# Kernel tuning notes

Measured on AMD Instinct MI355X. Metric: run time of the kernel, lower is better.

The kernel has to match this reference:

```python
import jax, jax.numpy as jnp
import numpy as np

B, V, CODE_NUM = 64, 100, 4096
CODE_SIZE, ATT, VISIT, TIME, HID, OUT = 256, 128, 256, 64, 512, 90
TYPE_NUM = 32
NEG = -2.0 ** 31


def setup_inputs() -> dict:
    key = jax.random.key(0)
    ks = jax.random.split(key, 24)
    s = 0.02
    return {
        'code_x': jax.random.randint(ks[0], (B, V, CODE_NUM), 0, 2).astype(jnp.float32),
        'code_type0': jax.random.randint(ks[1], (CODE_NUM + 1,), 0, TYPE_NUM),
        'code_type1': jax.random.randint(ks[2], (CODE_NUM + 1,), 0, TYPE_NUM),
        'code_type2': jax.random.randint(ks[3], (CODE_NUM + 1,), 0, TYPE_NUM),
        'lens': jax.random.randint(ks[4], (B,), 1, V + 1),
        'intervals': jax.random.uniform(ks[5], (B, V), dtype=jnp.float32),
        # encoder: code + 3 type embedding tables (rows 1..code_num used)
        'code_emb': jax.random.normal(ks[6], (CODE_NUM + 1, CODE_SIZE), jnp.float32) * s,
        't0_emb': jax.random.normal(ks[7], (TYPE_NUM, CODE_SIZE), jnp.float32) * s,
        't1_emb': jax.random.normal(ks[8], (TYPE_NUM, CODE_SIZE), jnp.float32) * s,
        't2_emb': jax.random.normal(ks[9], (TYPE_NUM, CODE_SIZE), jnp.float32) * s,
        # visit self-attention (no bias, per nn.Linear(..., bias=False))
        'Wq': jax.random.normal(ks[10], (CODE_SIZE, ATT), jnp.float32) * s,
        'Wk': jax.random.normal(ks[11], (CODE_SIZE, ATT), jnp.float32) * s,
        'Wv': jax.random.normal(ks[12], (CODE_SIZE, VISIT), jnp.float32) * s,
        # time embedding Linear(1, time_size)
        'time_w': jax.random.normal(ks[13], (TIME,), jnp.float32) * s,
        'time_b': jnp.zeros((TIME,), jnp.float32),
        # GRUCell params (torch layout: gates ordered r,z,n)
        'gru_Wih': jax.random.normal(ks[14], (3 * HID, VISIT + TIME), jnp.float32) * s,
        'gru_Whh': jax.random.normal(ks[15], (3 * HID, HID), jnp.float32) * s,
        'gru_bih': jnp.zeros((3 * HID,), jnp.float32),
        'gru_bhh': jnp.zeros((3 * HID,), jnp.float32),
        # classifier
        'cls_W': jax.random.normal(ks[16], (OUT, HID), jnp.float32) * s,
        'cls_b': jnp.zeros((OUT,), jnp.float32),
    }


def reference(code_x, code_type0, code_type1, code_type2, lens, intervals,
              code_emb, t0_emb, t1_emb, t2_emb, Wq, Wk, Wv, time_w, time_b,
              gru_Wih, gru_Whh, gru_bih, gru_bhh, cls_W, cls_b):
    # --- Encoder (vectorized): multi-hot slot i corresponds to code id i+1 ---
    E = (code_emb[1:]
         + t0_emb[code_type0[1:]]
         + t1_emb[code_type1[1:]]
         + t2_emb[code_type2[1:]])                      # [CODE_NUM, CODE_SIZE]
    active = (code_x > 0).astype(E.dtype)               # [B, V, CODE_NUM]
    counts = jnp.maximum(active.sum(-1, keepdims=True), 1.0)
    v_emb_ini = jnp.einsum('bvc,cd->bvd', active, E) / counts  # mean over codes
    visit_mask = jnp.arange(V)[None, :] < lens[:, None]        # [B, V]
    v_emb_ini = v_emb_ini * visit_mask[..., None]              # padded visits stay 0

    # --- Context-aware visit self-attention ---
    Q = v_emb_ini @ Wq                                   # [B, V, ATT]
    K = v_emb_ini @ Wk
    Vv = v_emb_ini @ Wv                                  # [B, V, VISIT]
    alpha = jnp.einsum('bqa,bka->bqk', Q, K)
    alpha = jnp.where(visit_mask[:, None, :], alpha, NEG)  # mask keys
    alpha = jax.nn.softmax(alpha, axis=2)
    v_emb = jnp.einsum('bqk,bkd->bqd', alpha, Vv) + Vv     # [B, V, VISIT]

    # --- Time-aware input ---
    t_emb = intervals[..., None] * time_w + time_b         # [B, V, TIME]
    x = jnp.concatenate([v_emb, t_emb], axis=-1)           # [B, V, VISIT+TIME]

    # --- GRU over visits, gated by per-patient length ---
    def step(h, xm):
        xt, mt = xm                                        # xt [B,D], mt [B]
        gi = xt @ gru_Wih.T + gru_bih
        gh = h @ gru_Whh.T + gru_bhh
        ir, iz, inn = jnp.split(gi, 3, axis=-1)
        hr, hz, hn = jnp.split(gh, 3, axis=-1)
        r = jax.nn.sigmoid(ir + hr)
        z = jax.nn.sigmoid(iz + hz)
        n = jnp.tanh(inn + r * hn)
        h_new = (1.0 - z) * n + z * h
        h = jnp.where(mt[:, None], h_new, h)
        return h, None

    h0 = jnp.zeros((B, HID), x.dtype)
    h_final, _ = jax.lax.scan(step, h0, (x.transpose(1, 0, 2), visit_mask.T))

    # --- Classifier (dropout p=0 -> identity) ---
    return jax.nn.sigmoid(h_final @ cls_W.T + cls_b)       # [B, OUT]
```

## Files before the change

### kernel.cpp

```cpp
#include <hip/hip_runtime.h>
#include <hip/hip_bf16.h>

typedef float  f32x4 __attribute__((ext_vector_type(4)));
typedef short  s16x8 __attribute__((ext_vector_type(8)));

#define NEGBIG -1e30f

__device__ __forceinline__ unsigned short f2b(float f) {
    union { float f; unsigned u; } c; c.f = f;
    unsigned r = c.u + 0x7FFF + ((c.u >> 16) & 1);
    return (unsigned short)(r >> 16);
}
__device__ __forceinline__ float b2f(unsigned short h) {
    union { unsigned u; float f; } c; c.u = ((unsigned)h) << 16;
    return c.f;
}
__device__ __forceinline__ float sigm(float x) { return 1.f / (1.f + __expf(-x)); }

__device__ __forceinline__ s16x8 ld_b128_sc(const unsigned short* p) {
    s16x8 r;
    asm volatile("global_load_dwordx4 %0, %1, off sc0 sc1" : "=v"(r) : "v"(p));
    return r;
}
__device__ __forceinline__ void st_short_sc(unsigned short* p, unsigned short v) {
    unsigned int dv = v;
    asm volatile("global_store_short %0, %1, off sc0 sc1" :: "v"(p), "v"(dv) : "memory");
}
__device__ __forceinline__ void st_dword_sc(float* p, float v) {
    asm volatile("global_store_dword %0, %1, off sc0 sc1" :: "v"(p), "v"(v) : "memory");
}

__global__ void init_zero(int* flags, unsigned short* hb0) {
    int t = threadIdx.x;
    for (int i = t; i < 1024; i += 256) flags[i] = 0;
    for (int i = t; i < 32768; i += 256) hb0[i] = 0;
}

__global__ void prep_w(const float* Wq, const float* Wk, const float* Wv,
                       const float* gWih, const float* gWhh,
                       unsigned short* wcat, unsigned short* wih, unsigned short* whh) {
    int idx = blockIdx.x * 256 + threadIdx.x;
    int stride = gridDim.x * 256;
    const int N1 = 131072, N2 = 491520, N3 = 786432;
    for (; idx < N1 + N2 + N3; idx += stride) {
        if (idx < N1) {
            int n = idx >> 8, k = idx & 255;
            float v;
            if (n < 128) v = Wq[k * 128 + n];
            else if (n < 256) v = Wk[k * 128 + (n - 128)];
            else v = Wv[k * 256 + (n - 256)];
            wcat[n * 256 + k] = f2b(v);
        } else if (idx < N1 + N2) {
            int i = idx - N1; wih[i] = f2b(gWih[i]);
        } else {
            int i = idx - N1 - N2; whh[i] = f2b(gWhh[i]);
        }
    }
}

__global__ __launch_bounds__(256) void prep_et(const float* code_emb, const int* ct0, const int* ct1, const int* ct2,
                                               const float* t0e, const float* t1e, const float* t2e,
                                               unsigned short* ET) {
    __shared__ float tile[64][65];
    const int d0 = blockIdx.x * 64, c0 = blockIdx.y * 64;
    const int t = threadIdx.x;
    for (int p = 0; p < 16; ++p) {
        int idx = p * 256 + t;
        int dl = idx & 63, cl = idx >> 6;
        int code = c0 + cl + 1;
        int d = d0 + dl;
        float v = code_emb[code * 256 + d] + t0e[ct0[code] * 256 + d]
                + t1e[ct1[code] * 256 + d] + t2e[ct2[code] * 256 + d];
        tile[dl][cl] = v;
    }
    __syncthreads();
    for (int p = 0; p < 2; ++p) {
        int idx = p * 256 + t;
        int dl = idx >> 3, ch = idx & 7;
        s16x8 pk;
#pragma unroll
        for (int e = 0; e < 8; ++e) pk[e] = (short)f2b(tile[dl][ch * 8 + e]);
        *(s16x8*)(ET + (size_t)(d0 + dl) * 4096 + c0 + ch * 8) = pk;
    }
}

__global__ __launch_bounds__(256) void enc_gemm(const float* code_x, const unsigned short* ET,
                                                const int* lens, unsigned short* Vb) {
    __shared__ __align__(16) char sm[4096 + 32768 + 128];
    char* As = sm;
    char* Bs = sm + 4096;
    float* cl = (float*)(sm + 4096 + 32768);
    const int m0 = blockIdx.x * 32;
    const int t = threadIdx.x, l = t & 63, w = t >> 6;
    const int lr = l & 15, lq = l >> 4, l7 = l & 7;
    const int sr = t >> 3, sc = t & 7;
    f32x4 acc[2][4];
#pragma unroll
    for (int a = 0; a < 2; ++a)
#pragma unroll
        for (int b = 0; b < 4; ++b) acc[a][b] = (f32x4){0.f, 0.f, 0.f, 0.f};
    int cnt = 0;
    for (int it = 0; it < 64; ++it) {
        const int k0 = it * 64;
        const float* ga = code_x + (size_t)(m0 + sr) * 4096 + k0 + sc * 8;
        f32x4 a0 = *(const f32x4*)ga;
        f32x4 a1 = *(const f32x4*)(ga + 4);
        s16x8 ap;
#pragma unroll
        for (int e = 0; e < 4; ++e) { bool on = a0[e] > 0.f; ap[e] = on ? (short)0x3F80 : (short)0; cnt += on ? 1 : 0; }
#pragma unroll
        for (int e = 0; e < 4; ++e) { bool on = a1[e] > 0.f; ap[4 + e] = on ? (short)0x3F80 : (short)0; cnt += on ? 1 : 0; }
        *(s16x8*)(As + sr * 128 + ((sc ^ (sr & 7)) << 4)) = ap;
#pragma unroll
        for (int rd = 0; rd < 8; ++rd) {
            int i = rd * 256 + t;
            int n = i >> 3, cc = i & 7;
            s16x8 bv = *(const s16x8*)(ET + (size_t)n * 4096 + k0 + cc * 8);
            *(s16x8*)(Bs + n * 128 + ((cc ^ (n & 7)) << 4)) = bv;
        }
        __syncthreads();
#pragma unroll
        for (int kk = 0; kk < 2; ++kk) {
            const int cp = kk * 4 + lq;
            s16x8 af[2], bf[4];
#pragma unroll
            for (int mt = 0; mt < 2; ++mt)
                af[mt] = *(const s16x8*)(As + (mt * 16 + lr) * 128 + ((cp ^ l7) << 4));
#pragma unroll
            for (int nt = 0; nt < 4; ++nt)
                bf[nt] = *(const s16x8*)(Bs + ((w * 4 + nt) * 16 + lr) * 128 + ((cp ^ l7) << 4));
#pragma unroll
            for (int mt = 0; mt < 2; ++mt)
#pragma unroll
                for (int nt = 0; nt < 4; ++nt)
                    acc[mt][nt] = __builtin_amdgcn_mfma_f32_16x16x32_bf16(af[mt], bf[nt], acc[mt][nt], 0, 0, 0);
        }
        __syncthreads();
    }
    float fc = (float)cnt;
    fc += __shfl_xor(fc, 1); fc += __shfl_xor(fc, 2); fc += __shfl_xor(fc, 4);
    if (sc == 0) cl[sr] = fmaxf(fc, 1.f);
    __syncthreads();
#pragma unroll
    for (int mt = 0; mt < 2; ++mt)
#pragma unroll
        for (int i = 0; i < 4; ++i) {
            int m = mt * 16 + lq * 4 + i;
            int gm = m0 + m;
            float rc = 1.f / cl[m];
            unsigned bi = (unsigned)gm / 100u;
            unsigned vi = (unsigned)gm - bi * 100u;
            float msk = ((int)vi < lens[bi]) ? 1.f : 0.f;
#pragma unroll
            for (int nt = 0; nt < 4; ++nt) {
                int n = (w * 4 + nt) * 16 + lr;
                Vb[(size_t)gm * 256 + n] = f2b(acc[mt][nt][i] * rc * msk);
            }
        }
}

__global__ __launch_bounds__(256) void gemm_bf16(const unsigned short* A, const unsigned short* Bm,
                                                 int K, int Ntot, int mode,
                                                 unsigned short* outp, const float* bias) {
    __shared__ __align__(16) char sm[4096 + 32768];
    char* As = sm;
    char* Bs = sm + 4096;
    const int m0 = blockIdx.x * 32;
    const int n0 = blockIdx.y * 256;
    const int t = threadIdx.x, l = t & 63, w = t >> 6;
    const int lr = l & 15, lq = l >> 4, l7 = l & 7;
    const int sr = t >> 3, sc = t & 7;
    const int iters = K >> 6;
    f32x4 acc[2][4];
#pragma unroll
    for (int a = 0; a < 2; ++a)
#pragma unroll
        for (int b = 0; b < 4; ++b) acc[a][b] = (f32x4){0.f, 0.f, 0.f, 0.f};
    for (int it = 0; it < iters; ++it) {
        const int k0 = it * 64;
        s16x8 av = *(const s16x8*)(A + (size_t)(m0 + sr) * K + k0 + sc * 8);
        *(s16x8*)(As + sr * 128 + ((sc ^ (sr & 7)) << 4)) = av;
#pragma unroll
        for (int rd = 0; rd < 8; ++rd) {
            int i = rd * 256 + t;
            int n = i >> 3, cc = i & 7;
            s16x8 bv = *(const s16x8*)(Bm + (size_t)(n0 + n) * K + k0 + cc * 8);
            *(s16x8*)(Bs + n * 128 + ((cc ^ (n & 7)) << 4)) = bv;
        }
        __syncthreads();
#pragma unroll
        for (int kk = 0; kk < 2; ++kk) {
            const int cp = kk * 4 + lq;
            s16x8 af[2], bf[4];
#pragma unroll
            for (int mt = 0; mt < 2; ++mt)
                af[mt] = *(const s16x8*)(As + (mt * 16 + lr) * 128 + ((cp ^ l7) << 4));
#pragma unroll
            for (int nt = 0; nt < 4; ++nt)
                bf[nt] = *(const s16x8*)(Bs + ((w * 4 + nt) * 16 + lr) * 128 + ((cp ^ l7) << 4));
#pragma unroll
            for (int mt = 0; mt < 2; ++mt)
#pragma unroll
                for (int nt = 0; nt < 4; ++nt)
                    acc[mt][nt] = __builtin_amdgcn_mfma_f32_16x16x32_bf16(af[mt], bf[nt], acc[mt][nt], 0, 0, 0);
        }
        __syncthreads();
    }
#pragma unroll
    for (int mt = 0; mt < 2; ++mt)
#pragma unroll
        for (int i = 0; i < 4; ++i) {
            int gm = m0 + mt * 16 + lq * 4 + i;
#pragma unroll
            for (int nt = 0; nt < 4; ++nt) {
                int n = n0 + (w * 4 + nt) * 16 + lr;
                float v = acc[mt][nt][i];
                if (mode == 1) v += bias[n];
                outp[(size_t)gm * Ntot + n] = f2b(v);
            }
        }
}

__global__ __launch_bounds__(256) void attn_kernel(const unsigned short* QKV, const int* lens,
                                                   const float* intervals, const float* time_w, const float* time_b,
                                                   unsigned short* X) {
    __shared__ __align__(16) char sm[28672 + 32768];
    char* Pb = sm;
    char* VTb = sm + 28672;
    const int b = blockIdx.x;
    const int t = threadIdx.x, l = t & 63, w = t >> 6;
    const int lr = l & 15, lq = l >> 4;
    const int lenb = lens[b];
    for (int p = 0; p < 7; ++p) {
        int idx = p * 256 + t;
        *(f32x4*)(Pb + idx * 16) = (f32x4){0.f, 0.f, 0.f, 0.f};
    }
    __syncthreads();
    f32x4 S[2][7];
#pragma unroll
    for (int a = 0; a < 2; ++a)
#pragma unroll
        for (int c = 0; c < 7; ++c) S[a][c] = (f32x4){0.f, 0.f, 0.f, 0.f};
#pragma unroll
    for (int kk = 0; kk < 4; ++kk) {
        s16x8 qa[2], kb[7];
#pragma unroll
        for (int mi = 0; mi < 2; ++mi) {
            int mt = 2 * w + mi;
            if (mt > 6) continue;
            int row = b * 100 + mt * 16 + lr;
            qa[mi] = *(const s16x8*)(QKV + (size_t)row * 512 + kk * 32 + lq * 8);
        }
#pragma unroll
        for (int nt = 0; nt < 7; ++nt) {
            int row = b * 100 + nt * 16 + lr;
            kb[nt] = *(const s16x8*)(QKV + (size_t)row * 512 + 128 + kk * 32 + lq * 8);
        }
#pragma unroll
        for (int mi = 0; mi < 2; ++mi) {
            int mt = 2 * w + mi;
            if (mt > 6) continue;
#pragma unroll
            for (int nt = 0; nt < 7; ++nt)
                S[mi][nt] = __builtin_amdgcn_mfma_f32_16x16x32_bf16(qa[mi], kb[nt], S[mi][nt], 0, 0, 0);
        }
    }
#pragma unroll
    for (int mi = 0; mi < 2; ++mi) {
        int mt = 2 * w + mi;
        if (mt > 6) continue;
        float sv[7][4];
#pragma unroll
        for (int nt = 0; nt < 7; ++nt) {
            int j = nt * 16 + lr;
#pragma unroll
            for (int i = 0; i < 4; ++i)
                sv[nt][i] = (j < lenb) ? S[mi][nt][i] : NEGBIG;
        }
#pragma unroll
        for (int i = 0; i < 4; ++i) {
            float mx = sv[0][i];
#pragma unroll
            for (int nt = 1; nt < 7; ++nt) mx = fmaxf(mx, sv[nt][i]);
            mx = fmaxf(mx, __shfl_xor(mx, 1));
            mx = fmaxf(mx, __shfl_xor(mx, 2));
            mx = fmaxf(mx, __shfl_xor(mx, 4));
            mx = fmaxf(mx, __shfl_xor(mx, 8));
            float e[7], sum = 0.f;
#pragma unroll
            for (int nt = 0; nt < 7; ++nt) { e[nt] = __expf(sv[nt][i] - mx); sum += e[nt]; }
            sum += __shfl_xor(sum, 1);
            sum += __shfl_xor(sum, 2);
            sum += __shfl_xor(sum, 4);
            sum += __shfl_xor(sum, 8);
            float rs = 1.f / sum;
            int m = mt * 16 + lq * 4 + i;
#pragma unroll
            for (int nt = 0; nt < 7; ++nt) {
                int j = nt * 16 + lr;
                *(unsigned short*)(Pb + m * 256 + (((j >> 3) ^ (m & 7)) << 4) + ((j & 7) << 1)) = f2b(e[nt] * rs);
            }
        }
    }
    __syncthreads();
    for (int h = 0; h < 2; ++h) {
        for (int p = 0; p < 8; ++p) {
            int idx = p * 256 + t;
            *(f32x4*)(VTb + idx * 16) = (f32x4){0.f, 0.f, 0.f, 0.f};
        }
        __syncthreads();
        for (int p = 0; p < 7; ++p) {
            int ci = p * 256 + t;
            if (ci < 1600) {
                int j = ci >> 4, d8 = ci & 15;
                s16x8 vv = *(const s16x8*)(QKV + (size_t)(b * 100 + j) * 512 + 256 + h * 128 + d8 * 8);
#pragma unroll
                for (int e = 0; e < 8; ++e) {
                    int dl = d8 * 8 + e;
                    *(unsigned short*)(VTb + dl * 256 + (((j >> 3) ^ (dl & 7)) << 4) + ((j & 7) << 1)) = (unsigned short)vv[e];
                }
            }
        }
        __syncthreads();
        f32x4 O[2][8];
#pragma unroll
        for (int a = 0; a < 2; ++a)
#pragma unroll
            for (int c = 0; c < 8; ++c) O[a][c] = (f32x4){0.f, 0.f, 0.f, 0.f};
#pragma unroll
        for (int kk = 0; kk < 4; ++kk) {
            s16x8 pa[2];
#pragma unroll
            for (int mi = 0; mi < 2; ++mi) {
                int mt = 2 * w + mi;
                if (mt > 6) continue;
                int m = mt * 16 + lr;
                pa[mi] = *(const s16x8*)(Pb + m * 256 + (((kk * 4 + lq) ^ (m & 7)) << 4));
            }
#pragma unroll
            for (int nt = 0; nt < 8; ++nt) {
                int dl = nt * 16 + lr;
                s16x8 vb = *(const s16x8*)(VTb + dl * 256 + (((kk * 4 + lq) ^ (dl & 7)) << 4));
#pragma unroll
                for (int mi = 0; mi < 2; ++mi) {
                    int mt = 2 * w + mi;
                    if (mt > 6) continue;
                    O[mi][nt] = __builtin_amdgcn_mfma_f32_16x16x32_bf16(pa[mi], vb, O[mi][nt], 0, 0, 0);
                }
            }
        }
#pragma unroll
        for (int mi = 0; mi < 2; ++mi) {
            int mt = 2 * w + mi;
            if (mt > 6) continue;
#pragma unroll
            for (int i = 0; i < 4; ++i) {
                int m = mt * 16 + lq * 4 + i;
                if (m < 100) {
#pragma unroll
                    for (int nt = 0; nt < 8; ++nt) {
                        int dl = nt * 16 + lr;
                        float res = b2f(*(unsigned short*)(VTb + dl * 256 + (((m >> 3) ^ (dl & 7)) << 4) + ((m & 7) << 1)));
                        X[(size_t)(b * 100 + m) * 320 + h * 128 + dl] = f2b(O[mi][nt][i] + res);
                    }
                }
            }
        }
        if (h == 0) __syncthreads();
    }
    for (int p = 0; p < 25; ++p) {
        int idx = p * 256 + t;
        int m = idx >> 6, d = idx & 63;
        float val = intervals[b * 100 + m] * time_w[d] + time_b[d];
        X[(size_t)(b * 100 + m) * 320 + 256 + d] = f2b(val);
    }
}

__global__ __launch_bounds__(256, 1) void gru_kernel(const unsigned short* GIb, const unsigned short* WHH,
                                                     const float* gbhh, const int* lens,
                                                     unsigned short* hb0, unsigned short* hb1, float* hf,
                                                     int* flags, const float* clsW, const float* clsb, float* out) {
    const int bid = blockIdx.x;
    const int t = threadIdx.x, l = t & 63, w = t >> 6;
    const int lr = l & 15, lq = l >> 4;
    const int d0 = bid * 16;
    const int j = d0 + lr;
    int ml;
    {
        int v = lens[l];
        v = max(v, __shfl_xor(v, 1));  v = max(v, __shfl_xor(v, 2));
        v = max(v, __shfl_xor(v, 4));  v = max(v, __shfl_xor(v, 8));
        v = max(v, __shfl_xor(v, 16)); v = max(v, __shfl_xor(v, 32));
        ml = v;
    }
    int lens4[4];
#pragma unroll
    for (int i = 0; i < 4; ++i) lens4[i] = lens[w * 16 + lq * 4 + i];
    const float bhr = gbhh[j], bhz = gbhh[512 + j], bhn = gbhh[1024 + j];
    s16x8 Bf[3][16];
#pragma unroll
    for (int g = 0; g < 3; ++g)
#pragma unroll
        for (int kk = 0; kk < 16; ++kk)
            Bf[g][kk] = *(const s16x8*)(WHH + (size_t)(g * 512 + j) * 512 + kk * 32 + lq * 8);
    float ho[4] = {0.f, 0.f, 0.f, 0.f};
    size_t gi_base[4];
#pragma unroll
    for (int i = 0; i < 4; ++i) gi_base[i] = (size_t)((w * 16 + lq * 4 + i) * 100) * 1536 + j;

    float gir[4], giz[4], gin[4];
#pragma unroll
    for (int i = 0; i < 4; ++i) {
        const unsigned short* gp = GIb + gi_base[i];
        gir[i] = b2f(gp[0]); giz[i] = b2f(gp[512]); gin[i] = b2f(gp[1024]);
    }

    for (int step = 0; step < ml; ++step) {
        const unsigned short* hb = (step & 1) ? hb1 : hb0;
        unsigned short* hn = (step & 1) ? hb0 : hb1;
        s16x8 af[16];
#pragma unroll
        for (int kk = 0; kk < 16; ++kk)
            af[kk] = ld_b128_sc(hb + (size_t)(w * 16 + lr) * 512 + kk * 32 + lq * 8);
        asm volatile("s_waitcnt vmcnt(0)" ::: "memory");
        __builtin_amdgcn_sched_barrier(0);
        f32x4 ar = (f32x4){0.f,0.f,0.f,0.f}, az = ar, an = ar;
#pragma unroll
        for (int kk = 0; kk < 16; ++kk) {
            ar = __builtin_amdgcn_mfma_f32_16x16x32_bf16(af[kk], Bf[0][kk], ar, 0, 0, 0);
            az = __builtin_amdgcn_mfma_f32_16x16x32_bf16(af[kk], Bf[1][kk], az, 0, 0, 0);
            an = __builtin_amdgcn_mfma_f32_16x16x32_bf16(af[kk], Bf[2][kk], an, 0, 0, 0);
        }
#pragma unroll
        for (int i = 0; i < 4; ++i) {
            float r = sigm(gir[i] + ar[i] + bhr);
            float z = sigm(giz[i] + az[i] + bhz);
            float n = tanhf(gin[i] + r * (an[i] + bhn));
            float hv = (step < lens4[i]) ? ((1.f - z) * n + z * ho[i]) : ho[i];
            ho[i] = hv;
            st_short_sc(hn + (size_t)(w * 16 + lq * 4 + i) * 512 + j, f2b(hv));
        }
        asm volatile("s_waitcnt vmcnt(0)" ::: "memory");
        __syncthreads();
        if (t == 0)
            __hip_atomic_store(flags + bid * 16, step + 1, __ATOMIC_RELAXED, __HIP_MEMORY_SCOPE_AGENT);
        if (step + 1 < ml) {
#pragma unroll
            for (int i = 0; i < 4; ++i) {
                const unsigned short* gp = GIb + gi_base[i] + (size_t)(step + 1) * 1536;
                gir[i] = b2f(gp[0]); giz[i] = b2f(gp[512]); gin[i] = b2f(gp[1024]);
            }
        }
        if (w == 0) {
            int guard = 0;
            while (true) {
                int v = (l < 32) ? __hip_atomic_load(flags + l * 16, __ATOMIC_RELAXED, __HIP_MEMORY_SCOPE_AGENT) : (step + 1);
                if (__all(v >= step + 1)) break;
                if (++guard > (1 << 20)) break;
                __builtin_amdgcn_s_sleep(1);
            }
        }
        __syncthreads();
    }
#pragma unroll
    for (int i = 0; i < 4; ++i)
        st_dword_sc(hf + (size_t)(w * 16 + lq * 4 + i) * 512 + j, ho[i]);
    asm volatile("s_waitcnt vmcnt(0)" ::: "memory");
    __syncthreads();
    if (t == 0)
        __hip_atomic_store(flags + bid * 16, ml + 1, __ATOMIC_RELAXED, __HIP_MEMORY_SCOPE_AGENT);
    if (w == 0) {
        int guard = 0;
        while (true) {
            int v = (l < 32) ? __hip_atomic_load(flags + l * 16, __ATOMIC_RELAXED, __HIP_MEMORY_SCOPE_AGENT) : (ml + 1);
            if (__all(v >= ml + 1)) break;
            if (++guard > (1 << 20)) break;
            __builtin_amdgcn_s_sleep(1);
        }
    }
    __syncthreads();
    if (bid < 30) {
        int bb = t >> 2, qq = t & 3;
        int c0 = bid * 3;
        float s0 = 0.f, s1 = 0.f, s2 = 0.f;
        for (int kc = 0; kc < 32; ++kc) {
            int k = qq * 128 + kc * 4;
            f32x4 hv = *(const f32x4*)(hf + bb * 512 + k);
            f32x4 w0 = *(const f32x4*)(clsW + (c0 + 0) * 512 + k);
            f32x4 w1 = *(const f32x4*)(clsW + (c0 + 1) * 512 + k);
            f32x4 w2 = *(const f32x4*)(clsW + (c0 + 2) * 512 + k);
            s0 += hv[0] * w0[0] + hv[1] * w0[1] + hv[2] * w0[2] + hv[3] * w0[3];
            s1 += hv[0] * w1[0] + hv[1] * w1[1] + hv[2] * w1[2] + hv[3] * w1[3];
            s2 += hv[0] * w2[0] + hv[1] * w2[1] + hv[2] * w2[2] + hv[3] * w2[3];
        }
        s0 += __shfl_xor(s0, 1); s0 += __shfl_xor(s0, 2);
        s1 += __shfl_xor(s1, 1); s1 += __shfl_xor(s1, 2);
        s2 += __shfl_xor(s2, 1); s2 += __shfl_xor(s2, 2);
        if (qq == 0) {
            out[bb * 90 + c0 + 0] = sigm(s0 + clsb[c0 + 0]);
            out[bb * 90 + c0 + 1] = sigm(s1 + clsb[c0 + 1]);
            out[bb * 90 + c0 + 2] = sigm(s2 + clsb[c0 + 2]);
        }
    }
}

extern "C" void kernel_launch(void* const* d_in, const int* in_sizes, int n_in,
                              void* d_out, int out_size, void* d_ws, size_t ws_size,
                              hipStream_t stream) {
    const float* code_x   = (const float*)d_in[0];
    const int*   ct0      = (const int*)d_in[1];
    const int*   ct1      = (const int*)d_in[2];
    const int*   ct2      = (const int*)d_in[3];
    const int*   lens     = (const int*)d_in[4];
    const float* intervals= (const float*)d_in[5];
    const float* code_emb = (const float*)d_in[6];
    const float* t0e      = (const float*)d_in[7];
    const float* t1e      = (const float*)d_in[8];
    const float* t2e      = (const float*)d_in[9];
    const float* Wq       = (const float*)d_in[10];
    const float* Wk       = (const float*)d_in[11];
    const float* Wv       = (const float*)d_in[12];
    const float* time_w   = (const float*)d_in[13];
    const float* time_b   = (const float*)d_in[14];
    const float* gWih     = (const float*)d_in[15];
    const float* gWhh     = (const float*)d_in[16];
    const float* gbih     = (const float*)d_in[17];
    const float* gbhh     = (const float*)d_in[18];
    const float* clsW     = (const float*)d_in[19];
    const float* clsb     = (const float*)d_in[20];

    char* ws = (char*)d_ws;
    const size_t ET_OFF   = 0;
    const size_t WCAT_OFF = 2097152;
    const size_t WIH_OFF  = 2359296;
    const size_t WHH_OFF  = 3342336;
    const size_t V_OFF    = 4915200;
    const size_t QKV_OFF  = 8192000;
    const size_t X_OFF    = 14778368;
    const size_t GI_OFF   = 18874368;
    const size_t HB0_OFF  = 38535168;
    const size_t HB1_OFF  = 38600704;
    const size_t HF_OFF   = 38666240;
    const size_t FLG_OFF  = 38797312;

    unsigned short* ET   = (unsigned short*)(ws + ET_OFF);
    unsigned short* WCAT = (unsigned short*)(ws + WCAT_OFF);
    unsigned short* WIH  = (unsigned short*)(ws + WIH_OFF);
    unsigned short* WHH  = (unsigned short*)(ws + WHH_OFF);
    unsigned short* Vb   = (unsigned short*)(ws + V_OFF);
    unsigned short* QKV  = (unsigned short*)(ws + QKV_OFF);
    unsigned short* Xb   = (unsigned short*)(ws + X_OFF);
    unsigned short* GIb  = (unsigned short*)(ws + GI_OFF);
    unsigned short* hb0  = (unsigned short*)(ws + HB0_OFF);
    unsigned short* hb1  = (unsigned short*)(ws + HB1_OFF);
    float*          hf   = (float*)(ws + HF_OFF);
    int*            flags= (int*)(ws + FLG_OFF);

    init_zero<<<1, 256, 0, stream>>>(flags, hb0);
    prep_w<<<512, 256, 0, stream>>>(Wq, Wk, Wv, gWih, gWhh, WCAT, WIH, WHH);
    prep_et<<<dim3(4, 64), 256, 0, stream>>>(code_emb, ct0, ct1, ct2, t0e, t1e, t2e, ET);
    enc_gemm<<<200, 256, 0, stream>>>(code_x, ET, lens, Vb);
    gemm_bf16<<<dim3(200, 2), 256, 0, stream>>>(Vb, WCAT, 256, 512, 2, QKV, nullptr);
    attn_kernel<<<64, 256, 0, stream>>>(QKV, lens, intervals, time_w, time_b, Xb);
    gemm_bf16<<<dim3(200, 6), 256, 0, stream>>>(Xb, WIH, 320, 1536, 1, GIb, gbih);
    gru_kernel<<<32, 256, 0, stream>>>(GIb, WHH, gbhh, lens, hb0, hb1, hf, flags, clsW, clsb, (float*)d_out);
}
```

Before: 769.9 us.

## Prefetch GEMM tiles into registers, merge prep kernels, split attention by head

```diff
diff --git a/kernel.cpp b/kernel.cpp
--- a/kernel.cpp
+++ b/kernel.cpp
@@ -30,57 +30,59 @@
     asm volatile("global_store_dword %0, %1, off sc0 sc1" :: "v"(p), "v"(v) : "memory");
 }
 
-__global__ void init_zero(int* flags, unsigned short* hb0) {
-    int t = threadIdx.x;
-    for (int i = t; i < 1024; i += 256) flags[i] = 0;
-    for (int i = t; i < 32768; i += 256) hb0[i] = 0;
-}
-
-__global__ void prep_w(const float* Wq, const float* Wk, const float* Wv,
-                       const float* gWih, const float* gWhh,
-                       unsigned short* wcat, unsigned short* wih, unsigned short* whh) {
-    int idx = blockIdx.x * 256 + threadIdx.x;
-    int stride = gridDim.x * 256;
-    const int N1 = 131072, N2 = 491520, N3 = 786432;
-    for (; idx < N1 + N2 + N3; idx += stride) {
-        if (idx < N1) {
-            int n = idx >> 8, k = idx & 255;
-            float v;
-            if (n < 128) v = Wq[k * 128 + n];
-            else if (n < 256) v = Wk[k * 128 + (n - 128)];
-            else v = Wv[k * 256 + (n - 256)];
-            wcat[n * 256 + k] = f2b(v);
-        } else if (idx < N1 + N2) {
-            int i = idx - N1; wih[i] = f2b(gWih[i]);
-        } else {
-            int i = idx - N1 - N2; whh[i] = f2b(gWhh[i]);
-        }
-    }
-}
-
-__global__ __launch_bounds__(256) void prep_et(const float* code_emb, const int* ct0, const int* ct1, const int* ct2,
-                                               const float* t0e, const float* t1e, const float* t2e,
-                                               unsigned short* ET) {
+__global__ __launch_bounds__(256) void prep_all(const float* code_emb, const int* ct0, const int* ct1, const int* ct2,
+                                                const float* t0e, const float* t1e, const float* t2e,
+                                                const float* Wq, const float* Wk, const float* Wv,
+                                                const float* gWih, const float* gWhh,
+                                                unsigned short* ET, unsigned short* wcat,
+                                                unsigned short* wih, unsigned short* whh,
+                                                int* flags, unsigned short* hb0) {
     __shared__ float tile[64][65];
-    const int d0 = blockIdx.x * 64, c0 = blockIdx.y * 64;
+    const int bid = blockIdx.x;
     const int t = threadIdx.x;
-    for (int p = 0; p < 16; ++p) {
-        int idx = p * 256 + t;
-        int dl = idx & 63, cl = idx >> 6;
-        int code = c0 + cl + 1;
-        int d = d0 + dl;
-        float v = code_emb[code * 256 + d] + t0e[ct0[code] * 256 + d]
-                + t1e[ct1[code] * 256 + d] + t2e[ct2[code] * 256 + d];
-        tile[dl][cl] = v;
-    }
-    __syncthreads();
-    for (int p = 0; p < 2; ++p) {
-        int idx = p * 256 + t;
-        int dl = idx >> 3, ch = idx & 7;
-        s16x8 pk;
-#pragma unroll
-        for (int e = 0; e < 8; ++e) pk[e] = (short)f2b(tile[dl][ch * 8 + e]);
-        *(s16x8*)(ET + (size_t)(d0 + dl) * 4096 + c0 + ch * 8) = pk;
+    if (bid < 256) {
+        const int d0 = (bid & 3) * 64, c0 = (bid >> 2) * 64;
+        for (int p = 0; p < 16; ++p) {
+            int idx = p * 256 + t;
+            int dl = idx & 63, cl = idx >> 6;
+            int code = c0 + cl + 1;
+            int d = d0 + dl;
+            float v = code_emb[code * 256 + d] + t0e[ct0[code] * 256 + d]
+                    + t1e[ct1[code] * 256 + d] + t2e[ct2[code] * 256 + d];
+            tile[dl][cl] = v;
+        }
+        __syncthreads();
+        for (int p = 0; p < 2; ++p) {
+            int idx = p * 256 + t;
+            int dl = idx >> 3, ch = idx & 7;
+            s16x8 pk;
+#pragma unroll
+            for (int e = 0; e < 8; ++e) pk[e] = (short)f2b(tile[dl][ch * 8 + e]);
+            *(s16x8*)(ET + (size_t)(d0 + dl) * 4096 + c0 + ch * 8) = pk;
+        }
+    } else {
+        if (bid >= 504) {
+            int idx = (bid - 504) * 256 + t;
+            for (int i = idx; i < 1024; i += 2048) flags[i] = 0;
+            for (int i = idx; i < 32768; i += 2048) hb0[i] = 0;
+        }
+        int idx = (bid - 256) * 256 + t;
+        const int stride = 256 * 256;
+        const int N1 = 131072, N2 = 491520, N3 = 786432;
+        for (; idx < N1 + N2 + N3; idx += stride) {
+            if (idx < N1) {
+                int n = idx >> 8, k = idx & 255;
+                float v;
+                if (n < 128) v = Wq[k * 128 + n];
+                else if (n < 256) v = Wk[k * 128 + (n - 128)];
+                else v = Wv[k * 256 + (n - 256)];
+                wcat[n * 256 + k] = f2b(v);
+            } else if (idx < N1 + N2) {
+                int i = idx - N1; wih[i] = f2b(gWih[i]);
+            } else {
+                int i = idx - N1 - N2; whh[i] = f2b(gWhh[i]);
+            }
+        }
     }
 }
 
@@ -94,49 +96,69 @@
     const int t = threadIdx.x, l = t & 63, w = t >> 6;
     const int lr = l & 15, lq = l >> 4, l7 = l & 7;
     const int sr = t >> 3, sc = t & 7;
+    const int bn = t >> 3, bc = t & 7;
+    const float* gabase = code_x + (size_t)(m0 + sr) * 4096 + sc * 8;
     f32x4 acc[2][4];
 #pragma unroll
     for (int a = 0; a < 2; ++a)
 #pragma unroll
         for (int b = 0; b < 4; ++b) acc[a][b] = (f32x4){0.f, 0.f, 0.f, 0.f};
     int cnt = 0;
-    for (int it = 0; it < 64; ++it) {
-        const int k0 = it * 64;
-        const float* ga = code_x + (size_t)(m0 + sr) * 4096 + k0 + sc * 8;
-        f32x4 a0 = *(const f32x4*)ga;
-        f32x4 a1 = *(const f32x4*)(ga + 4);
-        s16x8 ap;
-#pragma unroll
-        for (int e = 0; e < 4; ++e) { bool on = a0[e] > 0.f; ap[e] = on ? (short)0x3F80 : (short)0; cnt += on ? 1 : 0; }
-#pragma unroll
-        for (int e = 0; e < 4; ++e) { bool on = a1[e] > 0.f; ap[4 + e] = on ? (short)0x3F80 : (short)0; cnt += on ? 1 : 0; }
-        *(s16x8*)(As + sr * 128 + ((sc ^ (sr & 7)) << 4)) = ap;
-#pragma unroll
-        for (int rd = 0; rd < 8; ++rd) {
-            int i = rd * 256 + t;
-            int n = i >> 3, cc = i & 7;
-            s16x8 bv = *(const s16x8*)(ET + (size_t)n * 4096 + k0 + cc * 8);
-            *(s16x8*)(Bs + n * 128 + ((cc ^ (n & 7)) << 4)) = bv;
-        }
-        __syncthreads();
-#pragma unroll
-        for (int kk = 0; kk < 2; ++kk) {
-            const int cp = kk * 4 + lq;
-            s16x8 af[2], bf[4];
-#pragma unroll
-            for (int mt = 0; mt < 2; ++mt)
-                af[mt] = *(const s16x8*)(As + (mt * 16 + lr) * 128 + ((cp ^ l7) << 4));
-#pragma unroll
-            for (int nt = 0; nt < 4; ++nt)
-                bf[nt] = *(const s16x8*)(Bs + ((w * 4 + nt) * 16 + lr) * 128 + ((cp ^ l7) << 4));
-#pragma unroll
-            for (int mt = 0; mt < 2; ++mt)
-#pragma unroll
-                for (int nt = 0; nt < 4; ++nt)
-                    acc[mt][nt] = __builtin_amdgcn_mfma_f32_16x16x32_bf16(af[mt], bf[nt], acc[mt][nt], 0, 0, 0);
-        }
-        __syncthreads();
-    }
+
+    f32x4 a0A, a1A, a0B, a1B;
+    s16x8 bA[8], bB[8];
+
+#define ENC_ISSUE(SLOT, IT) do {                                                     \
+    const int k0_ = (IT) * 64;                                                       \
+    a0##SLOT = *(const f32x4*)(gabase + k0_);                                        \
+    a1##SLOT = *(const f32x4*)(gabase + k0_ + 4);                                    \
+    _Pragma("unroll")                                                                \
+    for (int rd_ = 0; rd_ < 8; ++rd_)                                                \
+        b##SLOT[rd_] = *(const s16x8*)(ET + (size_t)(rd_ * 32 + bn) * 4096 + k0_ + bc * 8); \
+} while (0)
+
+#define ENC_CONSUME(SLOT, NEXTIT) do {                                               \
+    s16x8 ap_;                                                                       \
+    _Pragma("unroll")                                                                \
+    for (int e_ = 0; e_ < 4; ++e_) { bool on_ = a0##SLOT[e_] > 0.f; ap_[e_] = on_ ? (short)0x3F80 : (short)0; cnt += on_ ? 1 : 0; } \
+    _Pragma("unroll")                                                                \
+    for (int e_ = 0; e_ < 4; ++e_) { bool on_ = a1##SLOT[e_] > 0.f; ap_[4 + e_] = on_ ? (short)0x3F80 : (short)0; cnt += on_ ? 1 : 0; } \
+    *(s16x8*)(As + sr * 128 + ((sc ^ (sr & 7)) << 4)) = ap_;                         \
+    _Pragma("unroll")                                                                \
+    for (int rd_ = 0; rd_ < 8; ++rd_) {                                              \
+        int n_ = rd_ * 32 + bn;                                                      \
+        *(s16x8*)(Bs + n_ * 128 + ((bc ^ (n_ & 7)) << 4)) = b##SLOT[rd_];            \
+    }                                                                                \
+    if ((NEXTIT) < 64) ENC_ISSUE(SLOT, NEXTIT);                                      \
+    __syncthreads();                                                                 \
+    _Pragma("unroll")                                                                \
+    for (int kk_ = 0; kk_ < 2; ++kk_) {                                              \
+        const int cp_ = kk_ * 4 + lq;                                                \
+        s16x8 af_[2], bf_[4];                                                        \
+        _Pragma("unroll")                                                            \
+        for (int mt_ = 0; mt_ < 2; ++mt_)                                            \
+            af_[mt_] = *(const s16x8*)(As + (mt_ * 16 + lr) * 128 + ((cp_ ^ l7) << 4)); \
+        _Pragma("unroll")                                                            \
+        for (int nt_ = 0; nt_ < 4; ++nt_)                                            \
+            bf_[nt_] = *(const s16x8*)(Bs + ((w * 4 + nt_) * 16 + lr) * 128 + ((cp_ ^ l7) << 4)); \
+        _Pragma("unroll")                                                            \
+        for (int mt_ = 0; mt_ < 2; ++mt_)                                            \
+            _Pragma("unroll")                                                        \
+            for (int nt_ = 0; nt_ < 4; ++nt_)                                        \
+                acc[mt_][nt_] = __builtin_amdgcn_mfma_f32_16x16x32_bf16(af_[mt_], bf_[nt_], acc[mt_][nt_], 0, 0, 0); \
+    }                                                                                \
+    __syncthreads();                                                                 \
+} while (0)
+
+    ENC_ISSUE(A, 0);
+    ENC_ISSUE(B, 1);
+    for (int base = 0; base < 64; base += 2) {
+        ENC_CONSUME(A, base + 2);
+        ENC_CONSUME(B, base + 3);
+    }
+#undef ENC_ISSUE
+#undef ENC_CONSUME
+
     float fc = (float)cnt;
     fc += __shfl_xor(fc, 1); fc += __shfl_xor(fc, 2); fc += __shfl_xor(fc, 4);
     if (sc == 0) cl[sr] = fmaxf(fc, 1.f);
@@ -170,42 +192,62 @@
     const int t = threadIdx.x, l = t & 63, w = t >> 6;
     const int lr = l & 15, lq = l >> 4, l7 = l & 7;
     const int sr = t >> 3, sc = t & 7;
+    const int bn = t >> 3, bc = t & 7;
     const int iters = K >> 6;
     f32x4 acc[2][4];
 #pragma unroll
     for (int a = 0; a < 2; ++a)
 #pragma unroll
         for (int b = 0; b < 4; ++b) acc[a][b] = (f32x4){0.f, 0.f, 0.f, 0.f};
-    for (int it = 0; it < iters; ++it) {
-        const int k0 = it * 64;
-        s16x8 av = *(const s16x8*)(A + (size_t)(m0 + sr) * K + k0 + sc * 8);
-        *(s16x8*)(As + sr * 128 + ((sc ^ (sr & 7)) << 4)) = av;
-#pragma unroll
-        for (int rd = 0; rd < 8; ++rd) {
-            int i = rd * 256 + t;
-            int n = i >> 3, cc = i & 7;
-            s16x8 bv = *(const s16x8*)(Bm + (size_t)(n0 + n) * K + k0 + cc * 8);
-            *(s16x8*)(Bs + n * 128 + ((cc ^ (n & 7)) << 4)) = bv;
-        }
-        __syncthreads();
-#pragma unroll
-        for (int kk = 0; kk < 2; ++kk) {
-            const int cp = kk * 4 + lq;
-            s16x8 af[2], bf[4];
-#pragma unroll
-            for (int mt = 0; mt < 2; ++mt)
-                af[mt] = *(const s16x8*)(As + (mt * 16 + lr) * 128 + ((cp ^ l7) << 4));
-#pragma unroll
-            for (int nt = 0; nt < 4; ++nt)
-                bf[nt] = *(const s16x8*)(Bs + ((w * 4 + nt) * 16 + lr) * 128 + ((cp ^ l7) << 4));
-#pragma unroll
-            for (int mt = 0; mt < 2; ++mt)
-#pragma unroll
-                for (int nt = 0; nt < 4; ++nt)
-                    acc[mt][nt] = __builtin_amdgcn_mfma_f32_16x16x32_bf16(af[mt], bf[nt], acc[mt][nt], 0, 0, 0);
-        }
-        __syncthreads();
-    }
+
+    s16x8 avA, avB;
+    s16x8 bA[8], bB[8];
+
+#define GB_ISSUE(SLOT, IT) do {                                                      \
+    const int k0_ = (IT) * 64;                                                       \
+    av##SLOT = *(const s16x8*)(A + (size_t)(m0 + sr) * K + k0_ + sc * 8);            \
+    _Pragma("unroll")                                                                \
+    for (int rd_ = 0; rd_ < 8; ++rd_)                                                \
+        b##SLOT[rd_] = *(const s16x8*)(Bm + (size_t)(n0 + rd_ * 32 + bn) * K + k0_ + bc * 8); \
+} while (0)
+
+#define GB_CONSUME(SLOT, NEXTIT) do {                                                \
+    *(s16x8*)(As + sr * 128 + ((sc ^ (sr & 7)) << 4)) = av##SLOT;                    \
+    _Pragma("unroll")                                                                \
+    for (int rd_ = 0; rd_ < 8; ++rd_) {                                              \
+        int n_ = rd_ * 32 + bn;                                                      \
+        *(s16x8*)(Bs + n_ * 128 + ((bc ^ (n_ & 7)) << 4)) = b##SLOT[rd_];            \
+    }                                                                                \
+    if ((NEXTIT) < iters) GB_ISSUE(SLOT, NEXTIT);                                    \
+    __syncthreads();                                                                 \
+    _Pragma("unroll")                                                                \
+    for (int kk_ = 0; kk_ < 2; ++kk_) {                                              \
+        const int cp_ = kk_ * 4 + lq;                                                \
+        s16x8 af_[2], bf_[4];                                                        \
+        _Pragma("unroll")                                                            \
+        for (int mt_ = 0; mt_ < 2; ++mt_)                                            \
+            af_[mt_] = *(const s16x8*)(As + (mt_ * 16 + lr) * 128 + ((cp_ ^ l7) << 4)); \
+        _Pragma("unroll")                                                            \
+        for (int nt_ = 0; nt_ < 4; ++nt_)                                            \
+            bf_[nt_] = *(const s16x8*)(Bs + ((w * 4 + nt_) * 16 + lr) * 128 + ((cp_ ^ l7) << 4)); \
+        _Pragma("unroll")                                                            \
+        for (int mt_ = 0; mt_ < 2; ++mt_)                                            \
+            _Pragma("unroll")                                                        \
+            for (int nt_ = 0; nt_ < 4; ++nt_)                                        \
+                acc[mt_][nt_] = __builtin_amdgcn_mfma_f32_16x16x32_bf16(af_[mt_], bf_[nt_], acc[mt_][nt_], 0, 0, 0); \
+    }                                                                                \
+    __syncthreads();                                                                 \
+} while (0)
+
+    GB_ISSUE(A, 0);
+    if (iters > 1) GB_ISSUE(B, 1);
+    for (int base = 0; base < iters; base += 2) {
+        GB_CONSUME(A, base + 2);
+        if (base + 1 < iters) GB_CONSUME(B, base + 3);
+    }
+#undef GB_ISSUE
+#undef GB_CONSUME
+
 #pragma unroll
     for (int mt = 0; mt < 2; ++mt)
 #pragma unroll
@@ -228,6 +270,7 @@
     char* Pb = sm;
     char* VTb = sm + 28672;
     const int b = blockIdx.x;
+    const int h = blockIdx.y;
     const int t = threadIdx.x, l = t & 63, w = t >> 6;
     const int lr = l & 15, lq = l >> 4;
     const int lenb = lens[b];
@@ -303,76 +346,75 @@
         }
     }
     __syncthreads();
-    for (int h = 0; h < 2; ++h) {
-        for (int p = 0; p < 8; ++p) {
-            int idx = p * 256 + t;
-            *(f32x4*)(VTb + idx * 16) = (f32x4){0.f, 0.f, 0.f, 0.f};
-        }
-        __syncthreads();
-        for (int p = 0; p < 7; ++p) {
-            int ci = p * 256 + t;
-            if (ci < 1600) {
-                int j = ci >> 4, d8 = ci & 15;
-                s16x8 vv = *(const s16x8*)(QKV + (size_t)(b * 100 + j) * 512 + 256 + h * 128 + d8 * 8);
-#pragma unroll
-                for (int e = 0; e < 8; ++e) {
-                    int dl = d8 * 8 + e;
-                    *(unsigned short*)(VTb + dl * 256 + (((j >> 3) ^ (dl & 7)) << 4) + ((j & 7) << 1)) = (unsigned short)vv[e];
-                }
-            }
-        }
-        __syncthreads();
-        f32x4 O[2][8];
-#pragma unroll
-        for (int a = 0; a < 2; ++a)
-#pragma unroll
-            for (int c = 0; c < 8; ++c) O[a][c] = (f32x4){0.f, 0.f, 0.f, 0.f};
-#pragma unroll
-        for (int kk = 0; kk < 4; ++kk) {
-            s16x8 pa[2];
+    for (int p = 0; p < 8; ++p) {
+        int idx = p * 256 + t;
+        *(f32x4*)(VTb + idx * 16) = (f32x4){0.f, 0.f, 0.f, 0.f};
+    }
+    __syncthreads();
+    for (int p = 0; p < 7; ++p) {
+        int ci = p * 256 + t;
+        if (ci < 1600) {
+            int j = ci >> 4, d8 = ci & 15;
+            s16x8 vv = *(const s16x8*)(QKV + (size_t)(b * 100 + j) * 512 + 256 + h * 128 + d8 * 8);
+#pragma unroll
+            for (int e = 0; e < 8; ++e) {
+                int dl = d8 * 8 + e;
+                *(unsigned short*)(VTb + dl * 256 + (((j >> 3) ^ (dl & 7)) << 4) + ((j & 7) << 1)) = (unsigned short)vv[e];
+            }
+        }
+    }
+    __syncthreads();
+    f32x4 O[2][8];
+#pragma unroll
+    for (int a = 0; a < 2; ++a)
+#pragma unroll
+        for (int c = 0; c < 8; ++c) O[a][c] = (f32x4){0.f, 0.f, 0.f, 0.f};
+#pragma unroll
+    for (int kk = 0; kk < 4; ++kk) {
+        s16x8 pa[2];
+#pragma unroll
+        for (int mi = 0; mi < 2; ++mi) {
+            int mt = 2 * w + mi;
+            if (mt > 6) continue;
+            int m = mt * 16 + lr;
+            pa[mi] = *(const s16x8*)(Pb + m * 256 + (((kk * 4 + lq) ^ (m & 7)) << 4));
+        }
+#pragma unroll
+        for (int nt = 0; nt < 8; ++nt) {
+            int dl = nt * 16 + lr;
+            s16x8 vb = *(const s16x8*)(VTb + dl * 256 + (((kk * 4 + lq) ^ (dl & 7)) << 4));
 #pragma unroll
             for (int mi = 0; mi < 2; ++mi) {
                 int mt = 2 * w + mi;
                 if (mt > 6) continue;
-                int m = mt * 16 + lr;
-                pa[mi] = *(const s16x8*)(Pb + m * 256 + (((kk * 4 + lq) ^ (m & 7)) << 4));
-            }
-#pragma unroll
-            for (int nt = 0; nt < 8; ++nt) {
-                int dl = nt * 16 + lr;
-                s16x8 vb = *(const s16x8*)(VTb + dl * 256 + (((kk * 4 + lq) ^ (dl & 7)) << 4));
-#pragma unroll
-                for (int mi = 0; mi < 2; ++mi) {
-                    int mt = 2 * w + mi;
-                    if (mt > 6) continue;
-                    O[mi][nt] = __builtin_amdgcn_mfma_f32_16x16x32_bf16(pa[mi], vb, O[mi][nt], 0, 0, 0);
+                O[mi][nt] = __builtin_amdgcn_mfma_f32_16x16x32_bf16(pa[mi], vb, O[mi][nt], 0, 0, 0);
+            }
+        }
+    }
+#pragma unroll
+    for (int mi = 0; mi < 2; ++mi) {
+        int mt = 2 * w + mi;
+        if (mt > 6) continue;
+#pragma unroll
+        for (int i = 0; i < 4; ++i) {
+            int m = mt * 16 + lq * 4 + i;
+            if (m < 100) {
+#pragma unroll
+                for (int nt = 0; nt < 8; ++nt) {
+                    int dl = nt * 16 + lr;
+                    float res = b2f(*(unsigned short*)(VTb + dl * 256 + (((m >> 3) ^ (dl & 7)) << 4) + ((m & 7) << 1)));
+                    X[(size_t)(b * 100 + m) * 320 + h * 128 + dl] = f2b(O[mi][nt][i] + res);
                 }
             }
         }
-#pragma unroll
-        for (int mi = 0; mi < 2; ++mi) {
-            int mt = 2 * w + mi;
-            if (mt > 6) continue;
-#pragma unroll
-            for (int i = 0; i < 4; ++i) {
-                int m = mt * 16 + lq * 4 + i;
-                if (m < 100) {
-#pragma unroll
-                    for (int nt = 0; nt < 8; ++nt) {
-                        int dl = nt * 16 + lr;
-                        float res = b2f(*(unsigned short*)(VTb + dl * 256 + (((m >> 3) ^ (dl & 7)) << 4) + ((m & 7) << 1)));
-                        X[(size_t)(b * 100 + m) * 320 + h * 128 + dl] = f2b(O[mi][nt][i] + res);
-                    }
-                }
-            }
-        }
-        if (h == 0) __syncthreads();
-    }
-    for (int p = 0; p < 25; ++p) {
-        int idx = p * 256 + t;
-        int m = idx >> 6, d = idx & 63;
-        float val = intervals[b * 100 + m] * time_w[d] + time_b[d];
-        X[(size_t)(b * 100 + m) * 320 + 256 + d] = f2b(val);
+    }
+    if (h == 0) {
+        for (int p = 0; p < 25; ++p) {
+            int idx = p * 256 + t;
+            int m = idx >> 6, d = idx & 63;
+            float val = intervals[b * 100 + m] * time_w[d] + time_b[d];
+            X[(size_t)(b * 100 + m) * 320 + 256 + d] = f2b(val);
+        }
     }
 }
 
@@ -556,12 +598,12 @@
     float*          hf   = (float*)(ws + HF_OFF);
     int*            flags= (int*)(ws + FLG_OFF);
 
-    init_zero<<<1, 256, 0, stream>>>(flags, hb0);
-    prep_w<<<512, 256, 0, stream>>>(Wq, Wk, Wv, gWih, gWhh, WCAT, WIH, WHH);
-    prep_et<<<dim3(4, 64), 256, 0, stream>>>(code_emb, ct0, ct1, ct2, t0e, t1e, t2e, ET);
+    prep_all<<<512, 256, 0, stream>>>(code_emb, ct0, ct1, ct2, t0e, t1e, t2e,
+                                      Wq, Wk, Wv, gWih, gWhh,
+                                      ET, WCAT, WIH, WHH, flags, hb0);
     enc_gemm<<<200, 256, 0, stream>>>(code_x, ET, lens, Vb);
     gemm_bf16<<<dim3(200, 2), 256, 0, stream>>>(Vb, WCAT, 256, 512, 2, QKV, nullptr);
-    attn_kernel<<<64, 256, 0, stream>>>(QKV, lens, intervals, time_w, time_b, Xb);
+    attn_kernel<<<dim3(64, 2), 256, 0, stream>>>(QKV, lens, intervals, time_w, time_b, Xb);
     gemm_bf16<<<dim3(200, 6), 256, 0, stream>>>(Xb, WIH, 320, 1536, 1, GIb, gbih);
     gru_kernel<<<32, 256, 0, stream>>>(GIb, WHH, gbhh, lens, hb0, hb1, hf, flags, clsW, clsb, (float*)d_out);
 }
```

New measurement: 728.7 us, median of 2. -5.4%, faster.
